# Performance work log

Measured on AMD Instinct MI355X. Metric: run time of the kernel, lower is better.

## Reference

```python
import jax, jax.numpy as jnp
import numpy as np

GAMMA = 10.0   # RBF width of the stand-in radial kernel
EPS = 1e-12    # safe-norm epsilon (avoids NaN grad at zero difference)

N_POINTS = 16384
N_NBR = 32
C_IN = 16
C_OUT = 16
N_BASIS = 16


def setup_inputs() -> dict:
    key = jax.random.key(0)
    k1, k2, k3, k4, k5, k6 = jax.random.split(key, 6)
    inp = jax.random.normal(k1, (C_IN, N_POINTS), dtype=jnp.float32)
    coords = jax.random.normal(k2, (N_POINTS, 3), dtype=jnp.float32)
    W = jax.random.normal(k3, (C_OUT, C_IN, N_BASIS), dtype=jnp.float32)
    centers = jax.random.uniform(k4, (N_BASIS,), dtype=jnp.float32)
    relative_mask = jax.random.uniform(k5, (N_POINTS, N_NBR), dtype=jnp.float32)
    neighbors = jax.random.randint(k6, (N_POINTS, N_NBR), 0, N_POINTS)
    return {"input": inp, "coords": coords, "W": W, "centers": centers,
            "relative_mask": relative_mask, "neighbors": neighbors}


def reference(input, coords, W, centers, relative_mask, neighbors):
    # difference_matrix: [N, K, 3]
    diff = coords[neighbors] - coords[:, None, :]
    # edge length with safe sqrt: [N, K]
    r = jnp.sqrt(jnp.sum(diff * diff, axis=-1) + EPS)
    # Gaussian radial basis: [N, K, B]
    rbf = jnp.exp(-GAMMA * (r[..., None] - centers) ** 2)
    # per-edge kernel: [C_out, C_in, N, K]
    kernel = jnp.einsum('oib,nkb->oink', W, rbf)
    # relative_mask applied as einsum 'ba,dcba->dcba'
    kernel = relative_mask * kernel
    # neighbor feature gather: [C_in, N, K]
    neighbors_input = input[:, neighbors]
    # contraction 'cba,dcba->db': [C_out, N]
    output = jnp.einsum('ink,oink->on', neighbors_input, kernel)
    return output
```

## Files before the change

### kernel.cpp

```cpp
#include <hip/hip_runtime.h>

#define NPTS 16384
#define NNBR 32
#define CIN 16
#define COUT 16
#define NBASIS 16

#define WF_OS 264
#define ML_PS 264

#define RSCL 3.7982825f

typedef _Float16 half8 __attribute__((ext_vector_type(8)));
typedef _Float16 half4 __attribute__((ext_vector_type(4)));
typedef unsigned short ushort8 __attribute__((ext_vector_type(8)));
typedef float floatx4 __attribute__((ext_vector_type(4)));

#define WS_XT 0
#define WS_WF (NPTS * CIN)

__global__ __launch_bounds__(256) void prep_kernel(
        const float* __restrict__ input, const float* __restrict__ W,
        _Float16* __restrict__ ws) {
    const int p4 = threadIdx.x >> 2;
    const int c4 = threadIdx.x & 3;
    const int n = blockIdx.x * 64 + p4;
    half4 v;
    #pragma unroll
    for (int j = 0; j < 4; ++j)
        v[j] = (_Float16)input[(c4 * 4 + j) * NPTS + n];
    *(half4*)&ws[WS_XT + n * CIN + c4 * 4] = v;
    if (blockIdx.x == 0) {
        const int o = threadIdx.x >> 4, b = threadIdx.x & 15;
        _Float16 w[16];
        #pragma unroll
        for (int i = 0; i < CIN; ++i) w[i] = (_Float16)W[o * 256 + i * 16 + b];
        *(half8*)&ws[WS_WF + o * 256 + b * 16]     = *(half8*)&w[0];
        *(half8*)&ws[WS_WF + o * 256 + b * 16 + 8] = *(half8*)&w[8];
    }
}

__global__ __launch_bounds__(256, 8) void se3_conv_kernel(
        const _Float16* __restrict__ ws,
        const float* __restrict__ coords,
        const float* __restrict__ centers,
        const float* __restrict__ mask,
        const int* __restrict__ neighbors,
        float* __restrict__ out) {
    __shared__ _Float16 Wf[COUT * WF_OS];
    __shared__ _Float16 Mld[8 * ML_PS];
    __shared__ float    rs[8 * NNBR];
    __shared__ unsigned short nb16[8 * NNBR];
    __shared__ _Float16 mv16[8 * NNBR];

    const _Float16* xT16 = &ws[WS_XT];

    const int tid = threadIdx.x;
    const int t = tid & 15;
    const int quad = (tid >> 4) & 3;
    const int wv = tid >> 6;
    const int nbase = blockIdx.x * 8;

    const int pt = tid >> 5;
    const int k = tid & 31;
    const int n = nbase + pt;
    const int nbr = neighbors[n * NNBR + k] & (NPTS - 1);
    const float m = mask[n * NNBR + k];
    const float nx = coords[n * 3 + 0], ny = coords[n * 3 + 1],
                nz = coords[n * 3 + 2];
    const float bx = coords[nbr * 3 + 0], by = coords[nbr * 3 + 1],
                bz = coords[nbr * 3 + 2];

    {
        const int o = tid >> 4, ch = tid & 15;
        const half8 w0 = *(const half8*)&ws[WS_WF + o * 256 + ch * 16];
        const half8 w1 = *(const half8*)&ws[WS_WF + o * 256 + ch * 16 + 8];
        *(half8*)&Wf[o * WF_OS + ch * 16]     = w0;
        *(half8*)&Wf[o * WF_OS + ch * 16 + 8] = w1;
    }

    {
        const float dx = bx - nx, dy = by - ny, dz = bz - nz;
        rs[pt * NNBR + k] =
            sqrtf(dx * dx + dy * dy + dz * dz + 1e-12f) * RSCL;
        nb16[pt * NNBR + k] = (unsigned short)nbr;
        mv16[pt * NNBR + k] = (_Float16)m;
    }

    const float cs = centers[t] * RSCL;
    const int kb0 = (wv * 2 + 0) * NNBR + 8 * quad;
    const int kb1 = (wv * 2 + 1) * NNBR + 8 * quad;
    const ushort8 nbv0 = *(const ushort8*)&nb16[kb0];
    const ushort8 nbv1 = *(const ushort8*)&nb16[kb1];
    const half8 mvv0 = *(const half8*)&mv16[kb0];
    const half8 mvv1 = *(const half8*)&mv16[kb1];
    const float4 r00 = *(const float4*)&rs[kb0];
    const float4 r01 = *(const float4*)&rs[kb0 + 4];
    const float4 r10 = *(const float4*)&rs[kb1];
    const float4 r11 = *(const float4*)&rs[kb1 + 4];

    half8 xh0, xh1;
    #pragma unroll
    for (int j = 0; j < 8; ++j) xh0[j] = xT16[(int)nbv0[j] * CIN + t];
    #pragma unroll
    for (int j = 0; j < 8; ++j) xh1[j] = xT16[(int)nbv1[j] * CIN + t];

    const float rj0[8] = {r00.x, r00.y, r00.z, r00.w, r01.x, r01.y, r01.z, r01.w};
    const float rj1[8] = {r10.x, r10.y, r10.z, r10.w, r11.x, r11.y, r11.z, r11.w};

    {
        half8 af, bf;
        #pragma unroll
        for (int j = 0; j < 8; ++j) {
            const float d = rj0[j] - cs;
            bf[j] = (_Float16)__builtin_amdgcn_exp2f(-(d * d));
        }
        af = xh0 * mvv0;
        floatx4 c = {0.0f, 0.0f, 0.0f, 0.0f};
        c = __builtin_amdgcn_mfma_f32_16x16x32_f16(af, bf, c, 0, 0, 0);
        _Float16 h[4];
        #pragma unroll
        for (int v = 0; v < 4; ++v) h[v] = (_Float16)c[v];
        *(uint2*)&Mld[(wv * 2 + 0) * ML_PS + t * 16 + 4 * quad] = *(uint2*)h;
    }
    {
        half8 af, bf;
        #pragma unroll
        for (int j = 0; j < 8; ++j) {
            const float d = rj1[j] - cs;
            bf[j] = (_Float16)__builtin_amdgcn_exp2f(-(d * d));
        }
        af = xh1 * mvv1;
        floatx4 c = {0.0f, 0.0f, 0.0f, 0.0f};
        c = __builtin_amdgcn_mfma_f32_16x16x32_f16(af, bf, c, 0, 0, 0);
        _Float16 h[4];
        #pragma unroll
        for (int v = 0; v < 4; ++v) h[v] = (_Float16)c[v];
        *(uint2*)&Mld[(wv * 2 + 1) * ML_PS + t * 16 + 4 * quad] = *(uint2*)h;
    }

    __syncthreads();

    floatx4 acc = {0.0f, 0.0f, 0.0f, 0.0f};
    #pragma unroll
    for (int cch = 0; cch < 8; ++cch) {
        const int bi = cch * 32 + 8 * quad;
        const half8 a = *(const half8*)&Wf[t * WF_OS + bi];
        half8 b = {};
        if (t < 8) b = *(const half8*)&Mld[t * ML_PS + bi];
        acc = __builtin_amdgcn_mfma_f32_16x16x32_f16(a, b, acc, 0, 0, 0);
    }
    if (t < 8 && wv == (t >> 1)) {
        #pragma unroll
        for (int v = 0; v < 4; ++v)
            out[(4 * quad + v) * NPTS + nbase + t] = acc[v];
    }
}

extern "C" void kernel_launch(void* const* d_in, const int* in_sizes, int n_in,
                              void* d_out, int out_size, void* d_ws, size_t ws_size,
                              hipStream_t stream) {
    const float* input   = (const float*)d_in[0];
    const float* coords  = (const float*)d_in[1];
    const float* W       = (const float*)d_in[2];
    const float* centers = (const float*)d_in[3];
    const float* mask    = (const float*)d_in[4];
    const int*   nbr     = (const int*)d_in[5];
    float* out = (float*)d_out;
    _Float16* ws = (_Float16*)d_ws;

    prep_kernel<<<NPTS / 64, 256, 0, stream>>>(input, W, ws);
    se3_conv_kernel<<<NPTS / 8, 256, 0, stream>>>(ws, coords, centers, mask,
                                                  nbr, out);
}
```

Before: 73.01 us.

## Vectorize neighbor feature gather via LDS staging and pad coords to float4

Neighbor features were fetched with 16 scattered 2-byte loads per lane. Now each wave fetches its neighbors' feature rows with two 16-byte loads per lane, stages them in a per-wave shared-memory tile, and reads the MFMA operands back from that tile. The prep kernel also writes coords out as padded float4, so each coordinate fetch becomes a single vector load instead of three scalar loads. This costs an extra workspace region and extra shared-memory traffic, and it relies on each wave's own writes to its shared-memory tile being ordered without an explicit barrier.

Result: no change. 74.33 us (+1.8%).

```diff
diff --git a/kernel.cpp b/kernel.cpp
--- a/kernel.cpp
+++ b/kernel.cpp
@@ -18,10 +18,11 @@
 
 #define WS_XT 0
 #define WS_WF (NPTS * CIN)
+#define WS_C4 (WS_WF + COUT * 256)
 
 __global__ __launch_bounds__(256) void prep_kernel(
-        const float* __restrict__ input, const float* __restrict__ W,
-        _Float16* __restrict__ ws) {
+        const float* __restrict__ input, const float* __restrict__ coords,
+        const float* __restrict__ W, _Float16* __restrict__ ws) {
     const int p4 = threadIdx.x >> 2;
     const int c4 = threadIdx.x & 3;
     const int n = blockIdx.x * 64 + p4;
@@ -30,6 +31,17 @@
     for (int j = 0; j < 4; ++j)
         v[j] = (_Float16)input[(c4 * 4 + j) * NPTS + n];
     *(half4*)&ws[WS_XT + n * CIN + c4 * 4] = v;
+
+    const int g = blockIdx.x * 256 + threadIdx.x;
+    if (g < NPTS) {
+        float4 cv;
+        cv.x = coords[3 * g + 0];
+        cv.y = coords[3 * g + 1];
+        cv.z = coords[3 * g + 2];
+        cv.w = 0.0f;
+        *(float4*)&((float*)&ws[WS_C4])[g * 4] = cv;
+    }
+
     if (blockIdx.x == 0) {
         const int o = threadIdx.x >> 4, b = threadIdx.x & 15;
         _Float16 w[16];
@@ -42,7 +54,6 @@
 
 __global__ __launch_bounds__(256, 8) void se3_conv_kernel(
         const _Float16* __restrict__ ws,
-        const float* __restrict__ coords,
         const float* __restrict__ centers,
         const float* __restrict__ mask,
         const int* __restrict__ neighbors,
@@ -52,13 +63,16 @@
     __shared__ float    rs[8 * NNBR];
     __shared__ unsigned short nb16[8 * NNBR];
     __shared__ _Float16 mv16[8 * NNBR];
+    __shared__ __align__(16) _Float16 Xld[4][NNBR * CIN];
 
     const _Float16* xT16 = &ws[WS_XT];
+    const float* c4 = (const float*)&ws[WS_C4];
 
     const int tid = threadIdx.x;
     const int t = tid & 15;
     const int quad = (tid >> 4) & 3;
     const int wv = tid >> 6;
+    const int lw = tid & 63;
     const int nbase = blockIdx.x * 8;
 
     const int pt = tid >> 5;
@@ -66,10 +80,8 @@
     const int n = nbase + pt;
     const int nbr = neighbors[n * NNBR + k] & (NPTS - 1);
     const float m = mask[n * NNBR + k];
-    const float nx = coords[n * 3 + 0], ny = coords[n * 3 + 1],
-                nz = coords[n * 3 + 2];
-    const float bx = coords[nbr * 3 + 0], by = coords[nbr * 3 + 1],
-                bz = coords[nbr * 3 + 2];
+    const float4 nc = *(const float4*)&c4[n * 4];
+    const float4 bc = *(const float4*)&c4[nbr * 4];
 
     {
         const int o = tid >> 4, ch = tid & 15;
@@ -80,30 +92,29 @@
     }
 
     {
-        const float dx = bx - nx, dy = by - ny, dz = bz - nz;
+        const float dx = bc.x - nc.x, dy = bc.y - nc.y, dz = bc.z - nc.z;
         rs[pt * NNBR + k] =
             sqrtf(dx * dx + dy * dy + dz * dz + 1e-12f) * RSCL;
         nb16[pt * NNBR + k] = (unsigned short)nbr;
         mv16[pt * NNBR + k] = (_Float16)m;
     }
 
+    const int rk = lw >> 1, hh = lw & 1;
+    const int sr0 = nb16[(2 * wv + 0) * NNBR + rk];
+    const int sr1 = nb16[(2 * wv + 1) * NNBR + rk];
+    const half8 g0 = *(const half8*)&xT16[sr0 * CIN + hh * 8];
+    const half8 g1 = *(const half8*)&xT16[sr1 * CIN + hh * 8];
+    *(half8*)&Xld[wv][rk * CIN + hh * 8] = g0;
+
     const float cs = centers[t] * RSCL;
     const int kb0 = (wv * 2 + 0) * NNBR + 8 * quad;
     const int kb1 = (wv * 2 + 1) * NNBR + 8 * quad;
-    const ushort8 nbv0 = *(const ushort8*)&nb16[kb0];
-    const ushort8 nbv1 = *(const ushort8*)&nb16[kb1];
     const half8 mvv0 = *(const half8*)&mv16[kb0];
     const half8 mvv1 = *(const half8*)&mv16[kb1];
     const float4 r00 = *(const float4*)&rs[kb0];
     const float4 r01 = *(const float4*)&rs[kb0 + 4];
     const float4 r10 = *(const float4*)&rs[kb1];
     const float4 r11 = *(const float4*)&rs[kb1 + 4];
-
-    half8 xh0, xh1;
-    #pragma unroll
-    for (int j = 0; j < 8; ++j) xh0[j] = xT16[(int)nbv0[j] * CIN + t];
-    #pragma unroll
-    for (int j = 0; j < 8; ++j) xh1[j] = xT16[(int)nbv1[j] * CIN + t];
 
     const float rj0[8] = {r00.x, r00.y, r00.z, r00.w, r01.x, r01.y, r01.z, r01.w};
     const float rj1[8] = {r10.x, r10.y, r10.z, r10.w, r11.x, r11.y, r11.z, r11.w};
@@ -112,10 +123,11 @@
         half8 af, bf;
         #pragma unroll
         for (int j = 0; j < 8; ++j) {
+            af[j] = Xld[wv][(8 * quad + j) * CIN + t];
             const float d = rj0[j] - cs;
             bf[j] = (_Float16)__builtin_amdgcn_exp2f(-(d * d));
         }
-        af = xh0 * mvv0;
+        af *= mvv0;
         floatx4 c = {0.0f, 0.0f, 0.0f, 0.0f};
         c = __builtin_amdgcn_mfma_f32_16x16x32_f16(af, bf, c, 0, 0, 0);
         _Float16 h[4];
@@ -123,14 +135,16 @@
         for (int v = 0; v < 4; ++v) h[v] = (_Float16)c[v];
         *(uint2*)&Mld[(wv * 2 + 0) * ML_PS + t * 16 + 4 * quad] = *(uint2*)h;
     }
+    *(half8*)&Xld[wv][rk * CIN + hh * 8] = g1;
     {
         half8 af, bf;
         #pragma unroll
         for (int j = 0; j < 8; ++j) {
+            af[j] = Xld[wv][(8 * quad + j) * CIN + t];
             const float d = rj1[j] - cs;
             bf[j] = (_Float16)__builtin_amdgcn_exp2f(-(d * d));
         }
-        af = xh1 * mvv1;
+        af *= mvv1;
         floatx4 c = {0.0f, 0.0f, 0.0f, 0.0f};
         c = __builtin_amdgcn_mfma_f32_16x16x32_f16(af, bf, c, 0, 0, 0);
         _Float16 h[4];
@@ -169,7 +183,6 @@
     float* out = (float*)d_out;
     _Float16* ws = (_Float16*)d_ws;
 
-    prep_kernel<<<NPTS / 64, 256, 0, stream>>>(input, W, ws);
-    se3_conv_kernel<<<NPTS / 8, 256, 0, stream>>>(ws, coords, centers, mask,
-                                                  nbr, out);
+    prep_kernel<<<NPTS / 64, 256, 0, stream>>>(input, coords, W, ws);
+    se3_conv_kernel<<<NPTS / 8, 256, 0, stream>>>(ws, centers, mask, nbr, out);
 }
```

## Process sixteen points per block to fill the second-stage MFMA

Applied to the files above, without the earlier changes.

Each block now handles 16 points instead of 8, so every thread computes per-edge data for two points and each wave runs four first-stage MFMAs instead of two. The second-stage MFMA now uses all 16 columns rather than zero-padding half of them, and the output store is spread across waves. This halves the grid, amortises the per-block weight staging, and removes the wasted MFMA work. In exchange it adds register and LDS pressure; occupancy hint drops to 4, leaving fewer blocks to hide gather latency.

Result: no change. 73.00 us (-0.0%).

```diff
diff --git a/kernel.cpp b/kernel.cpp
--- a/kernel.cpp
+++ b/kernel.cpp
@@ -40,7 +40,7 @@
     }
 }
 
-__global__ __launch_bounds__(256, 8) void se3_conv_kernel(
+__global__ __launch_bounds__(256, 4) void se3_conv_kernel(
         const _Float16* __restrict__ ws,
         const float* __restrict__ coords,
         const float* __restrict__ centers,
@@ -48,10 +48,10 @@
         const int* __restrict__ neighbors,
         float* __restrict__ out) {
     __shared__ _Float16 Wf[COUT * WF_OS];
-    __shared__ _Float16 Mld[8 * ML_PS];
-    __shared__ float    rs[8 * NNBR];
-    __shared__ unsigned short nb16[8 * NNBR];
-    __shared__ _Float16 mv16[8 * NNBR];
+    __shared__ _Float16 Mld[16 * ML_PS];
+    __shared__ float    rs[16 * NNBR];
+    __shared__ unsigned short nb16[16 * NNBR];
+    __shared__ _Float16 mv16[16 * NNBR];
 
     const _Float16* xT16 = &ws[WS_XT];
 
@@ -59,17 +59,23 @@
     const int t = tid & 15;
     const int quad = (tid >> 4) & 3;
     const int wv = tid >> 6;
-    const int nbase = blockIdx.x * 8;
-
+    const int nbase = blockIdx.x * 16;
     const int pt = tid >> 5;
     const int k = tid & 31;
-    const int n = nbase + pt;
-    const int nbr = neighbors[n * NNBR + k] & (NPTS - 1);
-    const float m = mask[n * NNBR + k];
-    const float nx = coords[n * 3 + 0], ny = coords[n * 3 + 1],
-                nz = coords[n * 3 + 2];
-    const float bx = coords[nbr * 3 + 0], by = coords[nbr * 3 + 1],
-                bz = coords[nbr * 3 + 2];
+
+    const int nA = nbase + pt, nB = nbase + 8 + pt;
+    const int nbrA = neighbors[nA * NNBR + k] & (NPTS - 1);
+    const int nbrB = neighbors[nB * NNBR + k] & (NPTS - 1);
+    const float mA = mask[nA * NNBR + k];
+    const float mB = mask[nB * NNBR + k];
+    const float nxA = coords[nA * 3 + 0], nyA = coords[nA * 3 + 1],
+                nzA = coords[nA * 3 + 2];
+    const float nxB = coords[nB * 3 + 0], nyB = coords[nB * 3 + 1],
+                nzB = coords[nB * 3 + 2];
+    const float bxA = coords[nbrA * 3 + 0], byA = coords[nbrA * 3 + 1],
+                bzA = coords[nbrA * 3 + 2];
+    const float bxB = coords[nbrB * 3 + 0], byB = coords[nbrB * 3 + 1],
+                bzB = coords[nbrB * 3 + 2];
 
     {
         const int o = tid >> 4, ch = tid & 15;
@@ -80,63 +86,115 @@
     }
 
     {
-        const float dx = bx - nx, dy = by - ny, dz = bz - nz;
+        const float dxA = bxA - nxA, dyA = byA - nyA, dzA = bzA - nzA;
         rs[pt * NNBR + k] =
-            sqrtf(dx * dx + dy * dy + dz * dz + 1e-12f) * RSCL;
-        nb16[pt * NNBR + k] = (unsigned short)nbr;
-        mv16[pt * NNBR + k] = (_Float16)m;
+            sqrtf(dxA * dxA + dyA * dyA + dzA * dzA + 1e-12f) * RSCL;
+        nb16[pt * NNBR + k] = (unsigned short)nbrA;
+        mv16[pt * NNBR + k] = (_Float16)mA;
+        const float dxB = bxB - nxB, dyB = byB - nyB, dzB = bzB - nzB;
+        rs[(8 + pt) * NNBR + k] =
+            sqrtf(dxB * dxB + dyB * dyB + dzB * dzB + 1e-12f) * RSCL;
+        nb16[(8 + pt) * NNBR + k] = (unsigned short)nbrB;
+        mv16[(8 + pt) * NNBR + k] = (_Float16)mB;
     }
 
     const float cs = centers[t] * RSCL;
-    const int kb0 = (wv * 2 + 0) * NNBR + 8 * quad;
-    const int kb1 = (wv * 2 + 1) * NNBR + 8 * quad;
-    const ushort8 nbv0 = *(const ushort8*)&nb16[kb0];
-    const ushort8 nbv1 = *(const ushort8*)&nb16[kb1];
-    const half8 mvv0 = *(const half8*)&mv16[kb0];
-    const half8 mvv1 = *(const half8*)&mv16[kb1];
-    const float4 r00 = *(const float4*)&rs[kb0];
-    const float4 r01 = *(const float4*)&rs[kb0 + 4];
-    const float4 r10 = *(const float4*)&rs[kb1];
-    const float4 r11 = *(const float4*)&rs[kb1 + 4];
-
-    half8 xh0, xh1;
-    #pragma unroll
-    for (int j = 0; j < 8; ++j) xh0[j] = xT16[(int)nbv0[j] * CIN + t];
-    #pragma unroll
-    for (int j = 0; j < 8; ++j) xh1[j] = xT16[(int)nbv1[j] * CIN + t];
-
-    const float rj0[8] = {r00.x, r00.y, r00.z, r00.w, r01.x, r01.y, r01.z, r01.w};
-    const float rj1[8] = {r10.x, r10.y, r10.z, r10.w, r11.x, r11.y, r11.z, r11.w};
-
-    {
-        half8 af, bf;
-        #pragma unroll
-        for (int j = 0; j < 8; ++j) {
-            const float d = rj0[j] - cs;
-            bf[j] = (_Float16)__builtin_amdgcn_exp2f(-(d * d));
-        }
-        af = xh0 * mvv0;
-        floatx4 c = {0.0f, 0.0f, 0.0f, 0.0f};
-        c = __builtin_amdgcn_mfma_f32_16x16x32_f16(af, bf, c, 0, 0, 0);
-        _Float16 h[4];
-        #pragma unroll
-        for (int v = 0; v < 4; ++v) h[v] = (_Float16)c[v];
-        *(uint2*)&Mld[(wv * 2 + 0) * ML_PS + t * 16 + 4 * quad] = *(uint2*)h;
-    }
-    {
-        half8 af, bf;
-        #pragma unroll
-        for (int j = 0; j < 8; ++j) {
-            const float d = rj1[j] - cs;
-            bf[j] = (_Float16)__builtin_amdgcn_exp2f(-(d * d));
-        }
-        af = xh1 * mvv1;
-        floatx4 c = {0.0f, 0.0f, 0.0f, 0.0f};
-        c = __builtin_amdgcn_mfma_f32_16x16x32_f16(af, bf, c, 0, 0, 0);
-        _Float16 h[4];
-        #pragma unroll
-        for (int v = 0; v < 4; ++v) h[v] = (_Float16)c[v];
-        *(uint2*)&Mld[(wv * 2 + 1) * ML_PS + t * 16 + 4 * quad] = *(uint2*)h;
+    const int pqA0 = 2 * wv, pqA1 = 2 * wv + 1;
+    const int pqB0 = 8 + 2 * wv, pqB1 = 9 + 2 * wv;
+    const int kbA0 = pqA0 * NNBR + 8 * quad;
+    const int kbA1 = pqA1 * NNBR + 8 * quad;
+    const int kbB0 = pqB0 * NNBR + 8 * quad;
+    const int kbB1 = pqB1 * NNBR + 8 * quad;
+    const ushort8 nvA0 = *(const ushort8*)&nb16[kbA0];
+    const ushort8 nvA1 = *(const ushort8*)&nb16[kbA1];
+    const ushort8 nvB0 = *(const ushort8*)&nb16[kbB0];
+    const ushort8 nvB1 = *(const ushort8*)&nb16[kbB1];
+
+    half8 xA0, xA1, xB0, xB1;
+    #pragma unroll
+    for (int j = 0; j < 8; ++j) xA0[j] = xT16[(int)nvA0[j] * CIN + t];
+    #pragma unroll
+    for (int j = 0; j < 8; ++j) xA1[j] = xT16[(int)nvA1[j] * CIN + t];
+    #pragma unroll
+    for (int j = 0; j < 8; ++j) xB0[j] = xT16[(int)nvB0[j] * CIN + t];
+    #pragma unroll
+    for (int j = 0; j < 8; ++j) xB1[j] = xT16[(int)nvB1[j] * CIN + t];
+
+    {
+        const half8 mvv = *(const half8*)&mv16[kbA0];
+        const float4 r0 = *(const float4*)&rs[kbA0];
+        const float4 r1 = *(const float4*)&rs[kbA0 + 4];
+        const float rj[8] = {r0.x, r0.y, r0.z, r0.w, r1.x, r1.y, r1.z, r1.w};
+        half8 af, bf;
+        #pragma unroll
+        for (int j = 0; j < 8; ++j) {
+            const float d = rj[j] - cs;
+            bf[j] = (_Float16)__builtin_amdgcn_exp2f(-(d * d));
+        }
+        af = xA0 * mvv;
+        floatx4 c = {0.0f, 0.0f, 0.0f, 0.0f};
+        c = __builtin_amdgcn_mfma_f32_16x16x32_f16(af, bf, c, 0, 0, 0);
+        _Float16 h[4];
+        #pragma unroll
+        for (int v = 0; v < 4; ++v) h[v] = (_Float16)c[v];
+        *(uint2*)&Mld[pqA0 * ML_PS + t * 16 + 4 * quad] = *(uint2*)h;
+    }
+    {
+        const half8 mvv = *(const half8*)&mv16[kbA1];
+        const float4 r0 = *(const float4*)&rs[kbA1];
+        const float4 r1 = *(const float4*)&rs[kbA1 + 4];
+        const float rj[8] = {r0.x, r0.y, r0.z, r0.w, r1.x, r1.y, r1.z, r1.w};
+        half8 af, bf;
+        #pragma unroll
+        for (int j = 0; j < 8; ++j) {
+            const float d = rj[j] - cs;
+            bf[j] = (_Float16)__builtin_amdgcn_exp2f(-(d * d));
+        }
+        af = xA1 * mvv;
+        floatx4 c = {0.0f, 0.0f, 0.0f, 0.0f};
+        c = __builtin_amdgcn_mfma_f32_16x16x32_f16(af, bf, c, 0, 0, 0);
+        _Float16 h[4];
+        #pragma unroll
+        for (int v = 0; v < 4; ++v) h[v] = (_Float16)c[v];
+        *(uint2*)&Mld[pqA1 * ML_PS + t * 16 + 4 * quad] = *(uint2*)h;
+    }
+    {
+        const half8 mvv = *(const half8*)&mv16[kbB0];
+        const float4 r0 = *(const float4*)&rs[kbB0];
+        const float4 r1 = *(const float4*)&rs[kbB0 + 4];
+        const float rj[8] = {r0.x, r0.y, r0.z, r0.w, r1.x, r1.y, r1.z, r1.w};
+        half8 af, bf;
+        #pragma unroll
+        for (int j = 0; j < 8; ++j) {
+            const float d = rj[j] - cs;
+            bf[j] = (_Float16)__builtin_amdgcn_exp2f(-(d * d));
+        }
+        af = xB0 * mvv;
+        floatx4 c = {0.0f, 0.0f, 0.0f, 0.0f};
+        c = __builtin_amdgcn_mfma_f32_16x16x32_f16(af, bf, c, 0, 0, 0);
+        _Float16 h[4];
+        #pragma unroll
+        for (int v = 0; v < 4; ++v) h[v] = (_Float16)c[v];
+        *(uint2*)&Mld[pqB0 * ML_PS + t * 16 + 4 * quad] = *(uint2*)h;
+    }
+    {
+        const half8 mvv = *(const half8*)&mv16[kbB1];
+        const float4 r0 = *(const float4*)&rs[kbB1];
+        const float4 r1 = *(const float4*)&rs[kbB1 + 4];
+        const float rj[8] = {r0.x, r0.y, r0.z, r0.w, r1.x, r1.y, r1.z, r1.w};
+        half8 af, bf;
+        #pragma unroll
+        for (int j = 0; j < 8; ++j) {
+            const float d = rj[j] - cs;
+            bf[j] = (_Float16)__builtin_amdgcn_exp2f(-(d * d));
+        }
+        af = xB1 * mvv;
+        floatx4 c = {0.0f, 0.0f, 0.0f, 0.0f};
+        c = __builtin_amdgcn_mfma_f32_16x16x32_f16(af, bf, c, 0, 0, 0);
+        _Float16 h[4];
+        #pragma unroll
+        for (int v = 0; v < 4; ++v) h[v] = (_Float16)c[v];
+        *(uint2*)&Mld[pqB1 * ML_PS + t * 16 + 4 * quad] = *(uint2*)h;
     }
 
     __syncthreads();
@@ -146,15 +204,10 @@
     for (int cch = 0; cch < 8; ++cch) {
         const int bi = cch * 32 + 8 * quad;
         const half8 a = *(const half8*)&Wf[t * WF_OS + bi];
-        half8 b = {};
-        if (t < 8) b = *(const half8*)&Mld[t * ML_PS + bi];
+        const half8 b = *(const half8*)&Mld[t * ML_PS + bi];
         acc = __builtin_amdgcn_mfma_f32_16x16x32_f16(a, b, acc, 0, 0, 0);
     }
-    if (t < 8 && wv == (t >> 1)) {
-        #pragma unroll
-        for (int v = 0; v < 4; ++v)
-            out[(4 * quad + v) * NPTS + nbase + t] = acc[v];
-    }
+    out[(4 * quad + wv) * NPTS + nbase + t] = acc[wv];
 }
 
 extern "C" void kernel_launch(void* const* d_in, const int* in_sizes, int n_in,
@@ -170,6 +223,6 @@
     _Float16* ws = (_Float16*)d_ws;
 
     prep_kernel<<<NPTS / 64, 256, 0, stream>>>(input, W, ws);
-    se3_conv_kernel<<<NPTS / 8, 256, 0, stream>>>(ws, coords, centers, mask,
-                                                  nbr, out);
+    se3_conv_kernel<<<NPTS / 16, 256, 0, stream>>>(ws, coords, centers, mask,
+                                                   nbr, out);
 }
```
